# Optimization experiments

Hardware: AMD Instinct MI355X
Metric: run time of the kernel (lower is better)

Reference implementation:

```python
import jax, jax.numpy as jnp
import numpy as np

N = 100000   # nodes
E = 1600000  # directed edges
D = 128      # feature dim (input = hidden = embedding)
LN_EPS = 1e-5


def setup_inputs() -> dict:
    key = jax.random.key(0)
    ks = jax.random.split(key, 8)
    scale = 1.0 / np.sqrt(D)
    x = jax.random.normal(ks[0], (N, D), dtype=jnp.float32)
    edge_index = jax.random.randint(ks[1], (2, E), 0, N, dtype=jnp.int64)
    W0 = jax.random.normal(ks[2], (D, D), dtype=jnp.float32) * scale
    W1 = jax.random.normal(ks[3], (D, D), dtype=jnp.float32) * scale
    W2 = jax.random.normal(ks[4], (D, D), dtype=jnp.float32) * scale
    b0 = jnp.zeros((D,), jnp.float32)
    b1 = jnp.zeros((D,), jnp.float32)
    b2 = jnp.zeros((D,), jnp.float32)
    ln_g = jnp.ones((D,), jnp.float32)
    ln_b = jnp.zeros((D,), jnp.float32)
    fn_g = jnp.ones((D,), jnp.float32)
    fn_b = jnp.zeros((D,), jnp.float32)
    return {"x": x, "edge_index": edge_index, "W0": W0, "b0": b0,
            "W1": W1, "b1": b1, "W2": W2, "b2": b2,
            "ln_g": ln_g, "ln_b": ln_b, "fn_g": fn_g, "fn_b": fn_b}


def _gcn_conv(x, W, b, src, dst, n):
    # PyG GCNConv: x' = D^{-1/2} (A + I) D^{-1/2} (x W) + b
    h = x @ W                                   # [N, D]
    # add self-loops
    loops = jnp.arange(n, dtype=src.dtype)
    s = jnp.concatenate([src, loops])           # source nodes
    d = jnp.concatenate([dst, loops])           # target nodes
    deg = jax.ops.segment_sum(jnp.ones_like(d, dtype=h.dtype), d, num_segments=n)
    dinv = jnp.where(deg > 0, jax.lax.rsqrt(deg), 0.0)
    norm = dinv[s] * dinv[d]                    # [E+N]
    msg = h[s] * norm[:, None]                  # gather + scale
    out = jax.ops.segment_sum(msg, d, num_segments=n)  # scatter-add at targets
    return out + b


def _layer_norm(x, g, b):
    mu = jnp.mean(x, axis=-1, keepdims=True)
    var = jnp.mean(jnp.square(x - mu), axis=-1, keepdims=True)
    return (x - mu) * jax.lax.rsqrt(var + LN_EPS) * g + b


def reference(x, edge_index, W0, b0, W1, b1, W2, b2, ln_g, ln_b, fn_g, fn_b):
    src, dst = edge_index[0], edge_index[1]
    n = x.shape[0]
    h = jax.nn.relu(_gcn_conv(x, W0, b0, src, dst, n))
    # single middle block (num_gnn_layers=3 -> loop runs for i=1 only)
    identity = h
    h = _layer_norm(h, ln_g, ln_b)
    h = jax.nn.relu(_gcn_conv(h, W1, b1, src, dst, n)) + identity
    h = _gcn_conv(h, W2, b2, src, dst, n)
    return _layer_norm(h, fn_g, fn_b)
```

## Files before the change

### kernel.cpp

```cpp
#include <hip/hip_runtime.h>
#include <hip/hip_bf16.h>

#define DIM 128
#define SB 256
#define NA 256
#define EAMAX 6272
#define BCAP 4096

typedef __attribute__((ext_vector_type(8))) short bf16x8;
typedef __attribute__((ext_vector_type(4))) float f32x4;

__device__ inline float bf2f(unsigned short u) {
    unsigned v = (unsigned)u << 16;
    union { unsigned u; float f; } c; c.u = v; return c.f;
}
__device__ inline unsigned short f2bf(float f) {
    union { __hip_bfloat16 h; unsigned short u; } c;
    c.h = __float2bfloat16(f);
    return c.u;
}
__device__ inline unsigned pk2(float a, float b) {
    return (unsigned)f2bf(a) | ((unsigned)f2bf(b) << 16);
}


__global__ __launch_bounds__(256) void k_hist(const int* __restrict__ dst,
                                              int* __restrict__ histG,
                                              int E, int EA, int nbuk) {
    __shared__ int h[1024];
    int t = threadIdx.x, blk = blockIdx.x;
    for (int i = t; i < 1024; i += 256) h[i] = 0;
    __syncthreads();
    int lo = blk * EA, hi = min(E, lo + EA);
    for (int i = lo + t; i < hi; i += 256) atomicAdd(&h[dst[i] >> 7], 1);
    __syncthreads();
    for (int bk = t; bk < nbuk; bk += 256) histG[bk * NA + blk] = h[bk];
}

__global__ __launch_bounds__(SB) void k_scan1(const int* __restrict__ cnt,
                                              int* __restrict__ bsum, int n) {
    int t = threadIdx.x;
    int i = blockIdx.x * SB + t;
    int v = (i < n) ? cnt[i] : 0;
#pragma unroll
    for (int m = 1; m < 64; m <<= 1) v += __shfl_xor(v, m);
    __shared__ int w[SB / 64];
    if ((t & 63) == 0) w[t >> 6] = v;
    __syncthreads();
    if (t == 0) {
        int s = 0;
#pragma unroll
        for (int k = 0; k < SB / 64; ++k) s += w[k];
        bsum[blockIdx.x] = s;
    }
}

__global__ __launch_bounds__(1024) void k_scan2(int* __restrict__ bsum, int B) {
    __shared__ int s[1024];
    int t = threadIdx.x;
    int v = (t < B) ? bsum[t] : 0;
    s[t] = v;
    __syncthreads();
    for (int off = 1; off < 1024; off <<= 1) {
        int u = (t >= off) ? s[t - off] : 0;
        __syncthreads();
        s[t] += u;
        __syncthreads();
    }
    if (t < B) bsum[t] = s[t] - v;
}

__global__ __launch_bounds__(SB) void k_scan3g(const int* __restrict__ cnt,
                                               const int* __restrict__ bsum,
                                               int* __restrict__ outx, int n) {
    __shared__ int s[SB];
    int t = threadIdx.x;
    int i = blockIdx.x * SB + t;
    int c = (i < n) ? cnt[i] : 0;
    s[t] = c;
    __syncthreads();
    for (int off = 1; off < SB; off <<= 1) {
        int u = (t >= off) ? s[t - off] : 0;
        __syncthreads();
        s[t] += u;
        __syncthreads();
    }
    int excl = bsum[blockIdx.x] + s[t] - c;
    if (i < n) {
        outx[i] = excl;
        if (i == n - 1) outx[n] = excl + c;
    }
}

__global__ __launch_bounds__(256) void k_place(const int* __restrict__ src,
                                               const int* __restrict__ dst,
                                               const int* __restrict__ scannedG,
                                               unsigned* __restrict__ ebuf,
                                               int E, int EA, int nbuk) {
    __shared__ int h[1024];
    __shared__ int dl[1024];
    __shared__ int ws4[4];
    __shared__ unsigned srt[EAMAX];
    __shared__ unsigned short bkt[EAMAX];
    int t = threadIdx.x, blk = blockIdx.x;
    int lo = blk * EA, hi = min(E, lo + EA);

    for (int i = t; i < 1024; i += 256) h[i] = 0;
    __syncthreads();
    for (int i = lo + t; i < hi; i += 256) atomicAdd(&h[dst[i] >> 7], 1);
    __syncthreads();

    {
        int b4 = t * 4;
        int v0 = h[b4], v1 = h[b4 + 1], v2 = h[b4 + 2], v3 = h[b4 + 3];
        int i1 = v0 + v1, i2 = i1 + v2, i3 = i2 + v3;
        int lane = t & 63, wv = t >> 6;
        int sc = i3;
#pragma unroll
        for (int o = 1; o < 64; o <<= 1) {
            int u = __shfl_up(sc, o);
            if (lane >= o) sc += u;
        }
        if (lane == 63) ws4[wv] = sc;
        __syncthreads();
        int woff = 0;
#pragma unroll
        for (int k = 0; k < 4; ++k) woff += (k < wv) ? ws4[k] : 0;
        int tex = woff + sc - i3;
        h[b4] = tex; h[b4 + 1] = tex + v0; h[b4 + 2] = tex + i1; h[b4 + 3] = tex + i2;
    }
    __syncthreads();

    for (int bk = t; bk < nbuk; bk += 256)
        dl[bk] = scannedG[bk * NA + blk] - h[bk];
    __syncthreads();

    for (int i = lo + t; i < hi; i += 256) {
        int d = dst[i];
        int bk = d >> 7;
        unsigned p = ((unsigned)(d & 127) << 17) | (unsigned)src[i];
        int r = atomicAdd(&h[bk], 1);
        srt[r] = p;
        bkt[r] = (unsigned short)bk;
    }
    __syncthreads();

    int m = hi - lo;
    for (int i = t; i < m; i += 256)
        ebuf[dl[bkt[i]] + i] = srt[i];
}

__global__ __launch_bounds__(256) void k_finish(const unsigned* __restrict__ ebuf,
                                                const int* __restrict__ scannedG,
                                                int* __restrict__ offs,
                                                float* __restrict__ dinv,
                                                int* __restrict__ csrc,
                                                int n, int nbuk) {
    __shared__ unsigned eds[BCAP];
    __shared__ unsigned srt[BCAP];
    __shared__ int lcnt[128], lcur[128];
    __shared__ int wsum[2];
    int b = blockIdx.x, t = threadIdx.x;
    int e0 = scannedG[b * NA], e1 = scannedG[(b + 1) * NA];
    int m = min(e1 - e0, BCAP);

    for (int i = t; i < m; i += 256) eds[i] = ebuf[e0 + i];
    if (t < 128) lcnt[t] = 0;
    __syncthreads();
    for (int i = t; i < m; i += 256) atomicAdd(&lcnt[eds[i] >> 17], 1);
    __syncthreads();

    int c = (t < 128) ? lcnt[t] : 0;
    int lane = t & 63, wv = t >> 6;
    int s = c;
#pragma unroll
    for (int o = 1; o < 64; o <<= 1) {
        int u = __shfl_up(s, o);
        if (lane >= o) s += u;
    }
    if (lane == 63 && wv < 2) wsum[wv] = s;
    __syncthreads();
    int excl = s - c + ((wv == 1) ? wsum[0] : 0);
    if (t < 128) {
        int node = b * 128 + t;
        if (node < n) {
            offs[node] = e0 + excl;
            dinv[node] = rsqrtf((float)(c + 1));
        }
        lcur[t] = excl;
    }
    if (b == nbuk - 1 && t == 0) offs[n] = e1;
    __syncthreads();

    for (int i = t; i < m; i += 256) {
        unsigned v = eds[i];
        int r = atomicAdd(&lcur[v >> 17], 1);
        srt[r] = v & 0x1FFFFu;
    }
    __syncthreads();
    for (int i = t; i < m; i += 256) csrc[e0 + i] = (int)srt[i];
}


__global__ __launch_bounds__(256) void k_gemm(const float* __restrict__ in,
                                              const float* __restrict__ W,
                                              const float* __restrict__ dinv,
                                              unsigned short* __restrict__ outH, int n) {
    __shared__ unsigned short Wt[DIM * 136];
    int t = threadIdx.x;
#pragma unroll
    for (int i = 0; i < 64; ++i) {
        int idx = i * 256 + t;
        int k = idx >> 7, nn = idx & 127;
        Wt[nn * 136 + k] = f2bf(W[idx]);
    }
    __syncthreads();

    int l = t & 63, w = t >> 6;
    int g = l >> 4, li = l & 15;
    int rbase = blockIdx.x * 128 + w * 32;

    f32x4 acc[2][8];
#pragma unroll
    for (int mt = 0; mt < 2; ++mt)
#pragma unroll
        for (int nt = 0; nt < 8; ++nt) acc[mt][nt] = (f32x4)(0.f);

#pragma unroll
    for (int kk = 0; kk < 4; ++kk) {
        bf16x8 a[2];
#pragma unroll
        for (int mt = 0; mt < 2; ++mt) {
            int row = rbase + mt * 16 + li;
            int rr = (row < n) ? row : (n - 1);
            const float* p = in + (size_t)rr * DIM + kk * 32 + g * 8;
            float4 v0 = *(const float4*)p;
            float4 v1 = *(const float4*)(p + 4);
            bf16x8 av;
            av[0] = (short)f2bf(v0.x); av[1] = (short)f2bf(v0.y);
            av[2] = (short)f2bf(v0.z); av[3] = (short)f2bf(v0.w);
            av[4] = (short)f2bf(v1.x); av[5] = (short)f2bf(v1.y);
            av[6] = (short)f2bf(v1.z); av[7] = (short)f2bf(v1.w);
            a[mt] = av;
        }
#pragma unroll
        for (int nt = 0; nt < 8; ++nt) {
            bf16x8 bb = *(const bf16x8*)&Wt[(nt * 16 + li) * 136 + kk * 32 + g * 8];
            acc[0][nt] = __builtin_amdgcn_mfma_f32_16x16x32_bf16(a[0], bb, acc[0][nt], 0, 0, 0);
            acc[1][nt] = __builtin_amdgcn_mfma_f32_16x16x32_bf16(a[1], bb, acc[1][nt], 0, 0, 0);
        }
    }

#pragma unroll
    for (int mt = 0; mt < 2; ++mt)
#pragma unroll
        for (int r = 0; r < 4; ++r) {
            int row = rbase + mt * 16 + g * 4 + r;
            if (row < n) {
                float s = dinv[row];
#pragma unroll
                for (int nt = 0; nt < 8; ++nt)
                    outH[(size_t)row * DIM + nt * 16 + li] = f2bf(acc[mt][nt][r] * s);
            }
        }
}


template <int MODE>
__global__ __launch_bounds__(256) void k_agg(const unsigned* __restrict__ H2,
                                             const float* __restrict__ dinv,
                                             const int* __restrict__ offs,
                                             const int* __restrict__ csrc,
                                             const float* __restrict__ bias,
                                             const float* __restrict__ identity,
                                             float* __restrict__ out_raw,
                                             float* __restrict__ out_ln,
                                             const float* __restrict__ lg,
                                             const float* __restrict__ lb, int n) {
    int wv = threadIdx.x >> 6, lane = threadIdx.x & 63;
    int i = blockIdx.x * 4 + wv;
    if (i >= n) return;

    unsigned u0 = H2[(size_t)i * 64 + lane];
    float ax = bf2f((unsigned short)(u0 & 0xffff));
    float ay = bf2f((unsigned short)(u0 >> 16));

    int s = offs[i], e = offs[i + 1];
    int j = s;
    for (; j + 16 <= e; j += 16) {
        int idx[16];
#pragma unroll
        for (int q = 0; q < 16; ++q) idx[q] = csrc[j + q];
        unsigned uu[16];
#pragma unroll
        for (int q = 0; q < 16; ++q) uu[q] = H2[(size_t)idx[q] * 64 + lane];
#pragma unroll
        for (int q = 0; q < 16; ++q) {
            ax += bf2f((unsigned short)(uu[q] & 0xffff));
            ay += bf2f((unsigned short)(uu[q] >> 16));
        }
    }
    for (; j + 4 <= e; j += 4) {
        unsigned uu[4];
#pragma unroll
        for (int q = 0; q < 4; ++q) uu[q] = H2[(size_t)csrc[j + q] * 64 + lane];
#pragma unroll
        for (int q = 0; q < 4; ++q) {
            ax += bf2f((unsigned short)(uu[q] & 0xffff));
            ay += bf2f((unsigned short)(uu[q] >> 16));
        }
    }
    for (; j < e; ++j) {
        unsigned v = H2[(size_t)csrc[j] * 64 + lane];
        ax += bf2f((unsigned short)(v & 0xffff));
        ay += bf2f((unsigned short)(v >> 16));
    }

    float di = dinv[i];
    float2 bs = ((const float2*)bias)[lane];
    float vx = di * ax + bs.x;
    float vy = di * ay + bs.y;

    float xx, xy;
    if (MODE == 0) { xx = fmaxf(vx, 0.f); xy = fmaxf(vy, 0.f); }
    if (MODE == 1) {
        float2 id = ((const float2*)(identity + (size_t)i * DIM))[lane];
        xx = fmaxf(vx, 0.f) + id.x;
        xy = fmaxf(vy, 0.f) + id.y;
    }
    if (MODE == 2) { xx = vx; xy = vy; }

    if (MODE == 0 || MODE == 1)
        ((float2*)(out_raw + (size_t)i * DIM))[lane] = make_float2(xx, xy);

    if (MODE == 0 || MODE == 2) {
        float su = xx + xy;
#pragma unroll
        for (int m = 1; m < 64; m <<= 1) su += __shfl_xor(su, m);
        float mu = su * (1.f / 128.f);
        float dx = xx - mu, dy = xy - mu;
        float q = dx * dx + dy * dy;
#pragma unroll
        for (int m = 1; m < 64; m <<= 1) q += __shfl_xor(q, m);
        float rstd = rsqrtf(q * (1.f / 128.f) + 1e-5f);
        float2 gg = ((const float2*)lg)[lane];
        float2 bb2 = ((const float2*)lb)[lane];
        ((float2*)(out_ln + (size_t)i * DIM))[lane] =
            make_float2(dx * rstd * gg.x + bb2.x, dy * rstd * gg.y + bb2.y);
    }
}


static inline char* alignp(char* p) {
    return (char*)(((size_t)p + 255) & ~(size_t)255);
}

extern "C" void kernel_launch(void* const* d_in, const int* in_sizes, int n_in,
                              void* d_out, int out_size, void* d_ws, size_t ws_size,
                              hipStream_t stream) {
    const float* x   = (const float*)d_in[0];
    const int*   ei  = (const int*)d_in[1];
    const float* W0  = (const float*)d_in[2];
    const float* b0  = (const float*)d_in[3];
    const float* W1  = (const float*)d_in[4];
    const float* b1  = (const float*)d_in[5];
    const float* W2  = (const float*)d_in[6];
    const float* b2  = (const float*)d_in[7];
    const float* lng = (const float*)d_in[8];
    const float* lnb = (const float*)d_in[9];
    const float* fng = (const float*)d_in[10];
    const float* fnb = (const float*)d_in[11];
    float* out = (float*)d_out;

    int n = in_sizes[0] / DIM;
    int E = in_sizes[1] / 2;
    const int* src = ei;
    const int* dst = ei + E;

    int nbuk = (n + 127) >> 7;
    int EA   = (E + NA - 1) / NA;
    int nh   = nbuk * NA;

    char* p = (char*)d_ws;
    unsigned short* H = (unsigned short*)p;  p = alignp(p + (size_t)n * DIM * 2);
    float* hb   = (float*)p;                 p = alignp(p + (size_t)n * DIM * 4);
    float* dinv = (float*)p;                 p = alignp(p + (size_t)n * 4);
    int*   offs = (int*)p;                   p = alignp(p + (size_t)(n + 1) * 4);
    int*   csrc = (int*)p;                   p = alignp(p + (size_t)E * 4);
    unsigned* ebuf = (unsigned*)p;           p = alignp(p + (size_t)E * 4);
    int*   histG = (int*)p;                  p = alignp(p + (size_t)nh * 4);
    int*   scannedG = (int*)p;               p = alignp(p + (size_t)(nh + 1) * 4);
    int*   bsum = (int*)p;

    int grid_g = (n + 127) / 128;
    int Bs = (nh + SB - 1) / SB;

    k_hist<<<NA, 256, 0, stream>>>(dst, histG, E, EA, nbuk);
    k_scan1<<<Bs, SB, 0, stream>>>(histG, bsum, nh);
    k_scan2<<<1, 1024, 0, stream>>>(bsum, Bs);
    k_scan3g<<<Bs, SB, 0, stream>>>(histG, bsum, scannedG, nh);
    k_place<<<NA, 256, 0, stream>>>(src, dst, scannedG, ebuf, E, EA, nbuk);
    k_finish<<<nbuk, 256, 0, stream>>>(ebuf, scannedG, offs, dinv, csrc, n, nbuk);

    const unsigned* H2 = (const unsigned*)H;
    int grid_a = (n + 3) / 4;

    k_gemm<<<grid_g, 256, 0, stream>>>(x, W0, dinv, H, n);
    k_agg<0><<<grid_a, 256, 0, stream>>>(H2, dinv, offs, csrc, b0, nullptr, hb, out, lng, lnb, n);

    k_gemm<<<grid_g, 256, 0, stream>>>(out, W1, dinv, H, n);
    k_agg<1><<<grid_a, 256, 0, stream>>>(H2, dinv, offs, csrc, b1, hb, hb, nullptr, nullptr, nullptr, n);

    k_gemm<<<grid_g, 256, 0, stream>>>(hb, W2, dinv, H, n);
    k_agg<2><<<grid_a, 256, 0, stream>>>(H2, dinv, offs, csrc, b2, nullptr, nullptr, out, fng, fnb, n);
}
```

Measured before the change: 347.1 us.

## Fuse neighbor aggregation with next layer's GEMM and shrink intermediates to bf16

Layers 1 and 2 now use a combined kernel: each block gathers and aggregates 32 nodes into a shared-memory bf16 tile, then multiplies it by the next layer's pre-transposed bf16 weights with MFMA. This removes the separate GEMM passes and their round trips of fp32 activations through global memory. The residual identity buffer is stored as bf16 instead of fp32, at some precision cost. The bucket-sum scan pass is replaced by atomics inside the histogram kernel, and the W1/W2 conversion moves to one small up-front kernel. The costs are a serial 8-nodes-per-wave gather and a per-block GEMM that reads weights straight from global memory.

```diff
diff --git a/kernel.cpp b/kernel.cpp
--- a/kernel.cpp
+++ b/kernel.cpp
@@ -26,6 +26,7 @@
 
 __global__ __launch_bounds__(256) void k_hist(const int* __restrict__ dst,
                                               int* __restrict__ histG,
+                                              int* __restrict__ bsum,
                                               int E, int EA, int nbuk) {
     __shared__ int h[1024];
     int t = threadIdx.x, blk = blockIdx.x;
@@ -34,24 +35,10 @@
     int lo = blk * EA, hi = min(E, lo + EA);
     for (int i = lo + t; i < hi; i += 256) atomicAdd(&h[dst[i] >> 7], 1);
     __syncthreads();
-    for (int bk = t; bk < nbuk; bk += 256) histG[bk * NA + blk] = h[bk];
-}
-
-__global__ __launch_bounds__(SB) void k_scan1(const int* __restrict__ cnt,
-                                              int* __restrict__ bsum, int n) {
-    int t = threadIdx.x;
-    int i = blockIdx.x * SB + t;
-    int v = (i < n) ? cnt[i] : 0;
-#pragma unroll
-    for (int m = 1; m < 64; m <<= 1) v += __shfl_xor(v, m);
-    __shared__ int w[SB / 64];
-    if ((t & 63) == 0) w[t >> 6] = v;
-    __syncthreads();
-    if (t == 0) {
-        int s = 0;
-#pragma unroll
-        for (int k = 0; k < SB / 64; ++k) s += w[k];
-        bsum[blockIdx.x] = s;
+    for (int bk = t; bk < nbuk; bk += 256) {
+        int c = h[bk];
+        histG[bk * NA + blk] = c;
+        if (c) atomicAdd(&bsum[bk], c);
     }
 }
 
@@ -202,10 +189,23 @@
 }
 
 
-__global__ __launch_bounds__(256) void k_gemm(const float* __restrict__ in,
-                                              const float* __restrict__ W,
-                                              const float* __restrict__ dinv,
-                                              unsigned short* __restrict__ outH, int n) {
+__global__ __launch_bounds__(256) void k_wcvt(const float* __restrict__ W1,
+                                              const float* __restrict__ W2,
+                                              unsigned short* __restrict__ o1,
+                                              unsigned short* __restrict__ o2) {
+    int idx = blockIdx.x * 256 + threadIdx.x;
+    if (idx < DIM * DIM) {
+        int k = idx >> 7, c = idx & 127;
+        o1[c * DIM + k] = f2bf(W1[idx]);
+        o2[c * DIM + k] = f2bf(W2[idx]);
+    }
+}
+
+
+__global__ __launch_bounds__(256) void k_gemm0(const float* __restrict__ inp,
+                                               const float* __restrict__ W,
+                                               const float* __restrict__ dinv,
+                                               unsigned short* __restrict__ outH, int n) {
     __shared__ unsigned short Wt[DIM * 136];
     int t = threadIdx.x;
 #pragma unroll
@@ -233,7 +233,7 @@
         for (int mt = 0; mt < 2; ++mt) {
             int row = rbase + mt * 16 + li;
             int rr = (row < n) ? row : (n - 1);
-            const float* p = in + (size_t)rr * DIM + kk * 32 + g * 8;
+            const float* p = inp + (size_t)rr * DIM + kk * 32 + g * 8;
             float4 v0 = *(const float4*)p;
             float4 v1 = *(const float4*)(p + 4);
             bf16x8 av;
@@ -267,16 +267,139 @@
 
 
 template <int MODE>
-__global__ __launch_bounds__(256) void k_agg(const unsigned* __restrict__ H2,
-                                             const float* __restrict__ dinv,
-                                             const int* __restrict__ offs,
-                                             const int* __restrict__ csrc,
-                                             const float* __restrict__ bias,
-                                             const float* __restrict__ identity,
-                                             float* __restrict__ out_raw,
-                                             float* __restrict__ out_ln,
-                                             const float* __restrict__ lg,
-                                             const float* __restrict__ lb, int n) {
+__global__ __launch_bounds__(256) void k_aggmm(const unsigned* __restrict__ H2,
+                                               const float* __restrict__ dinv,
+                                               const int* __restrict__ offs,
+                                               const int* __restrict__ csrc,
+                                               const float* __restrict__ bias,
+                                               const unsigned* __restrict__ idbf,
+                                               unsigned* __restrict__ hbout,
+                                               const float* __restrict__ lg,
+                                               const float* __restrict__ lb,
+                                               const unsigned short* __restrict__ WtG,
+                                               unsigned short* __restrict__ outH, int n) {
+    __shared__ unsigned At[32 * 68];
+    int t = threadIdx.x;
+    int w = t >> 6, lane = t & 63;
+    int base32 = blockIdx.x * 32;
+
+    for (int nn = 0; nn < 8; ++nn) {
+        int i = base32 + w * 8 + nn;
+        int rt = w * 8 + nn;
+        if (i < n) {
+            unsigned u0 = H2[(size_t)i * 64 + lane];
+            float ax = bf2f((unsigned short)(u0 & 0xffff));
+            float ay = bf2f((unsigned short)(u0 >> 16));
+
+            int s = offs[i], e = offs[i + 1];
+            int j = s;
+            for (; j + 16 <= e; j += 16) {
+                int idx[16];
+#pragma unroll
+                for (int q = 0; q < 16; ++q) idx[q] = csrc[j + q];
+                unsigned uu[16];
+#pragma unroll
+                for (int q = 0; q < 16; ++q) uu[q] = H2[(size_t)idx[q] * 64 + lane];
+#pragma unroll
+                for (int q = 0; q < 16; ++q) {
+                    ax += bf2f((unsigned short)(uu[q] & 0xffff));
+                    ay += bf2f((unsigned short)(uu[q] >> 16));
+                }
+            }
+            for (; j + 4 <= e; j += 4) {
+                unsigned uu[4];
+#pragma unroll
+                for (int q = 0; q < 4; ++q) uu[q] = H2[(size_t)csrc[j + q] * 64 + lane];
+#pragma unroll
+                for (int q = 0; q < 4; ++q) {
+                    ax += bf2f((unsigned short)(uu[q] & 0xffff));
+                    ay += bf2f((unsigned short)(uu[q] >> 16));
+                }
+            }
+            for (; j < e; ++j) {
+                unsigned v = H2[(size_t)csrc[j] * 64 + lane];
+                ax += bf2f((unsigned short)(v & 0xffff));
+                ay += bf2f((unsigned short)(v >> 16));
+            }
+
+            float di = dinv[i];
+            float2 bs = ((const float2*)bias)[lane];
+            float vx = di * ax + bs.x;
+            float vy = di * ay + bs.y;
+
+            if (MODE == 0) {
+                float xx = fmaxf(vx, 0.f), xy = fmaxf(vy, 0.f);
+                hbout[(size_t)i * 64 + lane] = pk2(xx, xy);
+                float su = xx + xy;
+#pragma unroll
+                for (int m = 1; m < 64; m <<= 1) su += __shfl_xor(su, m);
+                float mu = su * (1.f / 128.f);
+                float dx = xx - mu, dy = xy - mu;
+                float q = dx * dx + dy * dy;
+#pragma unroll
+                for (int m = 1; m < 64; m <<= 1) q += __shfl_xor(q, m);
+                float rstd = rsqrtf(q * (1.f / 128.f) + 1e-5f);
+                float2 gg = ((const float2*)lg)[lane];
+                float2 bb2 = ((const float2*)lb)[lane];
+                At[rt * 68 + lane] = pk2(dx * rstd * gg.x + bb2.x,
+                                         dy * rstd * gg.y + bb2.y);
+            } else {
+                unsigned idu = idbf[(size_t)i * 64 + lane];
+                float xx = fmaxf(vx, 0.f) + bf2f((unsigned short)(idu & 0xffff));
+                float xy = fmaxf(vy, 0.f) + bf2f((unsigned short)(idu >> 16));
+                At[rt * 68 + lane] = pk2(xx, xy);
+            }
+        } else {
+            At[rt * 68 + lane] = 0u;
+        }
+    }
+    __syncthreads();
+
+    int li = lane & 15, g4 = lane >> 4;
+    f32x4 acc[2][2];
+#pragma unroll
+    for (int mt = 0; mt < 2; ++mt)
+#pragma unroll
+        for (int nt = 0; nt < 2; ++nt) acc[mt][nt] = (f32x4)(0.f);
+
+#pragma unroll
+    for (int ks = 0; ks < 4; ++ks) {
+        bf16x8 a[2];
+#pragma unroll
+        for (int mt = 0; mt < 2; ++mt)
+            a[mt] = *(const bf16x8*)&At[(mt * 16 + li) * 68 + ks * 16 + g4 * 4];
+#pragma unroll
+        for (int nt = 0; nt < 2; ++nt) {
+            int col = w * 32 + nt * 16 + li;
+            bf16x8 bb = *(const bf16x8*)&WtG[(size_t)col * DIM + ks * 32 + g4 * 8];
+            acc[0][nt] = __builtin_amdgcn_mfma_f32_16x16x32_bf16(a[0], bb, acc[0][nt], 0, 0, 0);
+            acc[1][nt] = __builtin_amdgcn_mfma_f32_16x16x32_bf16(a[1], bb, acc[1][nt], 0, 0, 0);
+        }
+    }
+
+#pragma unroll
+    for (int mt = 0; mt < 2; ++mt)
+#pragma unroll
+        for (int r = 0; r < 4; ++r) {
+            int row = base32 + mt * 16 + g4 * 4 + r;
+            if (row < n) {
+                float s = dinv[row];
+#pragma unroll
+                for (int nt = 0; nt < 2; ++nt)
+                    outH[(size_t)row * DIM + w * 32 + nt * 16 + li] = f2bf(acc[mt][nt][r] * s);
+            }
+        }
+}
+
+
+__global__ __launch_bounds__(256) void k_aggln(const unsigned* __restrict__ H2,
+                                               const float* __restrict__ dinv,
+                                               const int* __restrict__ offs,
+                                               const int* __restrict__ csrc,
+                                               const float* __restrict__ bias,
+                                               float* __restrict__ outf,
+                                               const float* __restrict__ lg,
+                                               const float* __restrict__ lb, int n) {
     int wv = threadIdx.x >> 6, lane = threadIdx.x & 63;
     int i = blockIdx.x * 4 + wv;
     if (i >= n) return;
@@ -318,36 +441,22 @@
 
     float di = dinv[i];
     float2 bs = ((const float2*)bias)[lane];
-    float vx = di * ax + bs.x;
-    float vy = di * ay + bs.y;
-
-    float xx, xy;
-    if (MODE == 0) { xx = fmaxf(vx, 0.f); xy = fmaxf(vy, 0.f); }
-    if (MODE == 1) {
-        float2 id = ((const float2*)(identity + (size_t)i * DIM))[lane];
-        xx = fmaxf(vx, 0.f) + id.x;
-        xy = fmaxf(vy, 0.f) + id.y;
-    }
-    if (MODE == 2) { xx = vx; xy = vy; }
-
-    if (MODE == 0 || MODE == 1)
-        ((float2*)(out_raw + (size_t)i * DIM))[lane] = make_float2(xx, xy);
-
-    if (MODE == 0 || MODE == 2) {
-        float su = xx + xy;
-#pragma unroll
-        for (int m = 1; m < 64; m <<= 1) su += __shfl_xor(su, m);
-        float mu = su * (1.f / 128.f);
-        float dx = xx - mu, dy = xy - mu;
-        float q = dx * dx + dy * dy;
-#pragma unroll
-        for (int m = 1; m < 64; m <<= 1) q += __shfl_xor(q, m);
-        float rstd = rsqrtf(q * (1.f / 128.f) + 1e-5f);
-        float2 gg = ((const float2*)lg)[lane];
-        float2 bb2 = ((const float2*)lb)[lane];
-        ((float2*)(out_ln + (size_t)i * DIM))[lane] =
-            make_float2(dx * rstd * gg.x + bb2.x, dy * rstd * gg.y + bb2.y);
-    }
+    float xx = di * ax + bs.x;
+    float xy = di * ay + bs.y;
+
+    float su = xx + xy;
+#pragma unroll
+    for (int m = 1; m < 64; m <<= 1) su += __shfl_xor(su, m);
+    float mu = su * (1.f / 128.f);
+    float dx = xx - mu, dy = xy - mu;
+    float q = dx * dx + dy * dy;
+#pragma unroll
+    for (int m = 1; m < 64; m <<= 1) q += __shfl_xor(q, m);
+    float rstd = rsqrtf(q * (1.f / 128.f) + 1e-5f);
+    float2 gg = ((const float2*)lg)[lane];
+    float2 bb2 = ((const float2*)lb)[lane];
+    ((float2*)(outf + (size_t)i * DIM))[lane] =
+        make_float2(dx * rstd * gg.x + bb2.x, dy * rstd * gg.y + bb2.y);
 }
 
 
@@ -382,35 +491,42 @@
     int nh   = nbuk * NA;
 
     char* p = (char*)d_ws;
-    unsigned short* H = (unsigned short*)p;  p = alignp(p + (size_t)n * DIM * 2);
-    float* hb   = (float*)p;                 p = alignp(p + (size_t)n * DIM * 4);
+    unsigned short* HA = (unsigned short*)p; p = alignp(p + (size_t)n * DIM * 2);
+    unsigned short* HB = (unsigned short*)p; p = alignp(p + (size_t)n * DIM * 2);
+    unsigned* hb  = (unsigned*)p;            p = alignp(p + (size_t)n * DIM * 2);
     float* dinv = (float*)p;                 p = alignp(p + (size_t)n * 4);
     int*   offs = (int*)p;                   p = alignp(p + (size_t)(n + 1) * 4);
     int*   csrc = (int*)p;                   p = alignp(p + (size_t)E * 4);
     unsigned* ebuf = (unsigned*)p;           p = alignp(p + (size_t)E * 4);
     int*   histG = (int*)p;                  p = alignp(p + (size_t)nh * 4);
     int*   scannedG = (int*)p;               p = alignp(p + (size_t)(nh + 1) * 4);
-    int*   bsum = (int*)p;
+    int*   bsum = (int*)p;                   p = alignp(p + 1024 * 4);
+    unsigned short* Wt1g = (unsigned short*)p; p = alignp(p + DIM * DIM * 2);
+    unsigned short* Wt2g = (unsigned short*)p;
 
     int grid_g = (n + 127) / 128;
     int Bs = (nh + SB - 1) / SB;
 
-    k_hist<<<NA, 256, 0, stream>>>(dst, histG, E, EA, nbuk);
-    k_scan1<<<Bs, SB, 0, stream>>>(histG, bsum, nh);
-    k_scan2<<<1, 1024, 0, stream>>>(bsum, Bs);
+    k_wcvt<<<(DIM * DIM + 255) / 256, 256, 0, stream>>>(W1, W2, Wt1g, Wt2g);
+
+    hipMemsetAsync(bsum, 0, (size_t)nbuk * sizeof(int), stream);
+    k_hist<<<NA, 256, 0, stream>>>(dst, histG, bsum, E, EA, nbuk);
+    k_scan2<<<1, 1024, 0, stream>>>(bsum, nbuk);
     k_scan3g<<<Bs, SB, 0, stream>>>(histG, bsum, scannedG, nh);
     k_place<<<NA, 256, 0, stream>>>(src, dst, scannedG, ebuf, E, EA, nbuk);
     k_finish<<<nbuk, 256, 0, stream>>>(ebuf, scannedG, offs, dinv, csrc, n, nbuk);
 
-    const unsigned* H2 = (const unsigned*)H;
-    int grid_a = (n + 3) / 4;
-
-    k_gemm<<<grid_g, 256, 0, stream>>>(x, W0, dinv, H, n);
-    k_agg<0><<<grid_a, 256, 0, stream>>>(H2, dinv, offs, csrc, b0, nullptr, hb, out, lng, lnb, n);
-
-    k_gemm<<<grid_g, 256, 0, stream>>>(out, W1, dinv, H, n);
-    k_agg<1><<<grid_a, 256, 0, stream>>>(H2, dinv, offs, csrc, b1, hb, hb, nullptr, nullptr, nullptr, n);
-
-    k_gemm<<<grid_g, 256, 0, stream>>>(hb, W2, dinv, H, n);
-    k_agg<2><<<grid_a, 256, 0, stream>>>(H2, dinv, offs, csrc, b2, nullptr, nullptr, out, fng, fnb, n);
-}
+    int grid_m = (n + 31) / 32;
+    int grid_l = (n + 3) / 4;
+
+    k_gemm0<<<grid_g, 256, 0, stream>>>(x, W0, dinv, HA, n);
+
+    k_aggmm<0><<<grid_m, 256, 0, stream>>>((const unsigned*)HA, dinv, offs, csrc, b0,
+                                           nullptr, hb, lng, lnb, Wt1g, HB, n);
+
+    k_aggmm<1><<<grid_m, 256, 0, stream>>>((const unsigned*)HB, dinv, offs, csrc, b1,
+                                           hb, nullptr, nullptr, nullptr, Wt2g, HA, n);
+
+    k_aggln<<<grid_l, 256, 0, stream>>>((const unsigned*)HA, dinv, offs, csrc, b2,
+                                        out, fng, fnb, n);
+}
```

New measurement: 368.7 us. 6.2% more time.
